# Kernel optimization log

Measured on AMD Instinct MI355X. Metric: run time of the kernel, lower is better.

The kernel has to match this reference:

```python
import jax, jax.numpy as jnp
import numpy as np

N_NODES = 50000
EPS = 1e-5


def gcn_conv(x, edge_index, edge_weight, W, b, n):
    # PyG GCNConv: h = x @ W; out[dst] += norm * h[src]; out += b
    # with self-loops (weight 1) and symmetric normalization D^-1/2 A D^-1/2.
    src, dst = edge_index[0], edge_index[1]
    loop = jnp.arange(n)
    src_all = jnp.concatenate([src, loop])            # [E+N]
    dst_all = jnp.concatenate([dst, loop])
    w_all = jnp.concatenate([edge_weight, jnp.ones((n,), x.dtype)])
    deg = jax.ops.segment_sum(w_all, dst_all, num_segments=n)
    dinv = jnp.where(deg > 0, jax.lax.rsqrt(jnp.maximum(deg, 1e-30)), 0.0)
    norm = dinv[src_all] * w_all * dinv[dst_all]      # [E+N]
    h = x @ W                                         # [N, out]
    msg = h[src_all] * norm[:, None]                  # [E+N, out]
    return jax.ops.segment_sum(msg, dst_all, num_segments=n) + b


def setup_inputs() -> dict:
    key = jax.random.key(0)
    ks = jax.random.split(key, 8)
    nfeat, nhid, nout = 1024, 256, 256
    E = 800000
    x = jax.random.normal(ks[0], (N_NODES, nfeat), dtype=jnp.float32)
    edge_index = jax.random.randint(ks[1], (2, E), 0, N_NODES, dtype=jnp.int64)
    edge_weight = jax.random.uniform(ks[2], (E,), dtype=jnp.float32)
    W1 = jax.random.normal(ks[3], (nfeat, nhid), dtype=jnp.float32) / np.sqrt(nfeat)
    b1 = jnp.zeros((nhid,), jnp.float32)
    W2 = jax.random.normal(ks[4], (nhid, nout), dtype=jnp.float32) / np.sqrt(nhid)
    b2 = jnp.zeros((nout,), jnp.float32)
    bn_gamma = jnp.ones((nout,), jnp.float32)
    bn_beta = jnp.zeros((nout,), jnp.float32)
    ln_gamma = jnp.ones((nout,), jnp.float32)
    ln_beta = jnp.zeros((nout,), jnp.float32)
    return {"x": x, "edge_index": edge_index, "edge_weight": edge_weight,
            "W1": W1, "b1": b1, "W2": W2, "b2": b2,
            "bn_gamma": bn_gamma, "bn_beta": bn_beta,
            "ln_gamma": ln_gamma, "ln_beta": ln_beta}


def reference(x, edge_index, edge_weight, W1, b1, W2, b2,
              bn_gamma, bn_beta, ln_gamma, ln_beta):
    n = x.shape[0]
    # dropout is identity in eval mode
    h = jax.nn.relu(gcn_conv(x, edge_index, edge_weight, W1, b1, n))
    h = jax.nn.relu(gcn_conv(h, edge_index, edge_weight, W2, b2, n))
    # BatchNorm1d (training-mode batch statistics, biased variance)
    mu = jnp.mean(h, axis=0)
    var = jnp.mean((h - mu) ** 2, axis=0)
    h = (h - mu) * jax.lax.rsqrt(var + EPS) * bn_gamma + bn_beta
    # LayerNorm over feature dim
    lmu = jnp.mean(h, axis=-1, keepdims=True)
    lvar = jnp.mean((h - lmu) ** 2, axis=-1, keepdims=True)
    return (h - lmu) * jax.lax.rsqrt(lvar + EPS) * ln_gamma + ln_beta
```

## Files before the change

kernel.cpp:

```cpp
#include <hip/hip_runtime.h>


typedef __attribute__((ext_vector_type(4))) float f32x4;
typedef __attribute__((ext_vector_type(8))) _Float16 f16x8;
typedef __attribute__((ext_vector_type(4))) _Float16 f16x4;

#define NN 50000
#define NF 1024
#define NH 256

__global__ __launch_bounds__(256) void deg_count(const int* __restrict__ ei,
    const float* __restrict__ ew, float* __restrict__ deg, int* __restrict__ cnt, int E)
{
    int e = blockIdx.x * 256 + threadIdx.x;
    if (e >= E) return;
    int d = ei[E + e];
    atomicAdd(&deg[d], ew[e]);
    atomicAdd(&cnt[d], 1);
}

__global__ __launch_bounds__(256) void dinv_k(const float* __restrict__ deg,
    float* __restrict__ dinv, int n)
{
    int i = blockIdx.x * 256 + threadIdx.x;
    if (i < n) dinv[i] = rsqrtf(deg[i] + 1.0f);
}

__global__ __launch_bounds__(512) void scan_a(const int* __restrict__ cnt,
    int* __restrict__ excl, int* __restrict__ bsum, int n)
{
    __shared__ int sm[512];
    int t = threadIdx.x, g = blockIdx.x * 512 + t;
    int v = (g < n) ? cnt[g] : 0;
    sm[t] = v;
    __syncthreads();
    for (int d = 1; d < 512; d <<= 1) {
        int x = (t >= d) ? sm[t - d] : 0;
        __syncthreads();
        sm[t] += x;
        __syncthreads();
    }
    if (g < n) excl[g] = sm[t] - v;
    if (t == 511) bsum[blockIdx.x] = sm[511];
}

__global__ __launch_bounds__(128) void scan_b(int* __restrict__ bsum, int nb)
{
    __shared__ int sm[128];
    int t = threadIdx.x;
    int v = (t < nb) ? bsum[t] : 0;
    sm[t] = v;
    __syncthreads();
    for (int d = 1; d < 128; d <<= 1) {
        int x = (t >= d) ? sm[t - d] : 0;
        __syncthreads();
        sm[t] += x;
        __syncthreads();
    }
    if (t < nb) bsum[t] = sm[t] - v;
}

__global__ __launch_bounds__(256) void scan_c(const int* __restrict__ excl,
    const int* __restrict__ bsum, int* __restrict__ offs, int n, int E)
{
    int g = blockIdx.x * 256 + threadIdx.x;
    if (g < n) offs[g] = excl[g] + bsum[g >> 9];
    else if (g == n) offs[n] = E;
}

__global__ __launch_bounds__(256) void scatter_k(const int* __restrict__ ei,
    const float* __restrict__ ew, const int* __restrict__ offs,
    int* __restrict__ cursor, const float* __restrict__ dinv,
    int* __restrict__ csrc, float* __restrict__ cwv, int E)
{
    int e = blockIdx.x * 256 + threadIdx.x;
    if (e >= E) return;
    int s = ei[e], d = ei[E + e];
    int pos = offs[d] + atomicAdd(&cursor[d], 1);
    csrc[pos] = s;
    cwv[pos] = ew[e] * dinv[s] * dinv[d];
}

__global__ __launch_bounds__(256) void cvt_w(const float* __restrict__ W,
    unsigned short* __restrict__ WT, int K, int total)
{
    int idx = blockIdx.x * 256 + threadIdx.x;
    if (idx >= total) return;
    int k = idx >> 8, n = idx & 255;
    ((_Float16*)WT)[(size_t)n * K + k] = (_Float16)W[idx];
}

template<bool AF32>
__global__ __launch_bounds__(256) void gemm_mfma(
    const void* __restrict__ Av, const unsigned short* __restrict__ BT,
    _Float16* __restrict__ C, int M, int K)
{
    constexpr int AS = AF32 ? 40 : 32;
    __shared__ _Float16 As[2][128 * AS];
    __shared__ _Float16 Bs[2][128 * 32];
    const int t = threadIdx.x;
    const int lane = t & 63, wid = t >> 6;
    const int r = lane & 15, q = lane >> 4;
    const int n0 = blockIdx.x * 128;
    const int m0 = blockIdx.y * 128;
    const int wm = (wid >> 1) * 64, wn = (wid & 1) * 64;
    const float* Af = (const float*)Av;
    const _Float16* Ah = (const _Float16*)Av;

    f32x4 acc[4][4];
#pragma unroll
    for (int i = 0; i < 4; ++i)
#pragma unroll
        for (int j = 0; j < 4; ++j) acc[i][j] = (f32x4){0.f, 0.f, 0.f, 0.f};

    const int T = K >> 5;
    float4 a_pre[4];

    if constexpr (AF32) {
#pragma unroll
        for (int it = 0; it < 4; ++it) {
            int f = it * 256 + t;
            int m = f >> 3, kc = (f & 7) << 2;
            int gm = m0 + m; if (gm >= M) gm = M - 1;
            a_pre[it] = *(const float4*)(Af + (size_t)gm * K + kc);
        }
    } else {
#pragma unroll
        for (int rd = 0; rd < 2; ++rd) {
            int row = rd * 64 + (t >> 2), kc = (t & 3) << 3;
            int gm = m0 + row; if (gm >= M) gm = M - 1;
            const _Float16* g = Ah + (size_t)gm * K + kc;
            _Float16* l = &As[0][0] + rd * 2048 + wid * 512;
            __builtin_amdgcn_global_load_lds(
                (const __attribute__((address_space(1))) unsigned int*)g,
                (__attribute__((address_space(3))) unsigned int*)l, 16, 0, 0);
        }
    }
#pragma unroll
    for (int rd = 0; rd < 2; ++rd) {
        int c = rd * 256 + t;
        int n = c >> 2, kc = (c & 3) << 3;
        const _Float16* g = (const _Float16*)BT + (size_t)(n0 + n) * K + kc;
        _Float16* l = &Bs[0][0] + rd * 2048 + wid * 512;
        __builtin_amdgcn_global_load_lds(
            (const __attribute__((address_space(1))) unsigned int*)g,
            (__attribute__((address_space(3))) unsigned int*)l, 16, 0, 0);
    }

    for (int k = 0; k < T; ++k) {
        const int cur = k & 1, nxt = cur ^ 1;
        if constexpr (AF32) {
#pragma unroll
            for (int it = 0; it < 4; ++it) {
                int f = it * 256 + t;
                int m = f >> 3, kc = (f & 7) << 2;
                f16x4 hv;
                hv.x = (_Float16)a_pre[it].x; hv.y = (_Float16)a_pre[it].y;
                hv.z = (_Float16)a_pre[it].z; hv.w = (_Float16)a_pre[it].w;
                *(f16x4*)(&As[cur][0] + m * AS + kc) = hv;
            }
        }
        __syncthreads();

        if (k + 1 < T) {
            const int k1 = (k + 1) << 5;
#pragma unroll
            for (int rd = 0; rd < 2; ++rd) {
                int c = rd * 256 + t;
                int n = c >> 2, kc = (c & 3) << 3;
                const _Float16* g = (const _Float16*)BT + (size_t)(n0 + n) * K + k1 + kc;
                _Float16* l = &Bs[nxt][0] + rd * 2048 + wid * 512;
                __builtin_amdgcn_global_load_lds(
                    (const __attribute__((address_space(1))) unsigned int*)g,
                    (__attribute__((address_space(3))) unsigned int*)l, 16, 0, 0);
            }
            if constexpr (AF32) {
#pragma unroll
                for (int it = 0; it < 4; ++it) {
                    int f = it * 256 + t;
                    int m = f >> 3, kc = (f & 7) << 2;
                    int gm = m0 + m; if (gm >= M) gm = M - 1;
                    a_pre[it] = *(const float4*)(Af + (size_t)gm * K + k1 + kc);
                }
            } else {
#pragma unroll
                for (int rd = 0; rd < 2; ++rd) {
                    int row = rd * 64 + (t >> 2), kc = (t & 3) << 3;
                    int gm = m0 + row; if (gm >= M) gm = M - 1;
                    const _Float16* g = Ah + (size_t)gm * K + k1 + kc;
                    _Float16* l = &As[nxt][0] + rd * 2048 + wid * 512;
                    __builtin_amdgcn_global_load_lds(
                        (const __attribute__((address_space(1))) unsigned int*)g,
                        (__attribute__((address_space(3))) unsigned int*)l, 16, 0, 0);
                }
            }
        }

        f16x8 af[4], bfr[4];
#pragma unroll
        for (int i = 0; i < 4; ++i)
            af[i] = *(const f16x8*)(&As[cur][0] + (wm + i * 16 + r) * AS + q * 8);
#pragma unroll
        for (int j = 0; j < 4; ++j)
            bfr[j] = *(const f16x8*)(&Bs[cur][0] + (wn + j * 16 + r) * 32 + q * 8);
#pragma unroll
        for (int i = 0; i < 4; ++i)
#pragma unroll
            for (int j = 0; j < 4; ++j)
                acc[i][j] = __builtin_amdgcn_mfma_f32_16x16x32_f16(af[i], bfr[j], acc[i][j], 0, 0, 0);
    }

#pragma unroll
    for (int i = 0; i < 4; ++i) {
#pragma unroll
        for (int reg = 0; reg < 4; ++reg) {
            int m = m0 + wm + i * 16 + q * 4 + reg;
            if (m < M) {
                _Float16* cp = C + (size_t)m * 256 + (n0 + wn + r);
#pragma unroll
                for (int j = 0; j < 4; ++j) cp[j * 16] = (_Float16)acc[i][j][reg];
            }
        }
    }
}

__global__ __launch_bounds__(256) void agg_relu(
    const _Float16* __restrict__ h, const int* __restrict__ roff,
    const int* __restrict__ csrc, const float* __restrict__ cwv,
    const float* __restrict__ dinv, const float* __restrict__ bias,
    _Float16* __restrict__ out, int n)
{
    const int lane = threadIdx.x & 63, wid = threadIdx.x >> 6;
    const int i = blockIdx.x * 4 + wid;
    if (i >= n) return;
    const int c = lane << 2;
    const float di = dinv[i];
    const float sw = di * di;
    const f16x4 hv = *(const f16x4*)(h + (size_t)i * 256 + c);
    float a0 = sw * (float)hv.x, a1 = sw * (float)hv.y;
    float a2 = sw * (float)hv.z, a3 = sw * (float)hv.w;
    float c0 = 0.f, c1 = 0.f, c2 = 0.f, c3 = 0.f;
    const int p0 = roff[i], pe = roff[i + 1];
    for (int base = p0; base < pe; base += 64) {
        int lim = pe - base; if (lim > 64) lim = 64;
        int sv = 0; float wv = 0.f;
        if (lane < lim) { sv = csrc[base + lane]; wv = cwv[base + lane]; }
        int j = 0;
        for (; j + 1 < lim; j += 2) {
            int s0 = __shfl(sv, j), s1 = __shfl(sv, j + 1);
            float w0 = __shfl(wv, j), w1 = __shfl(wv, j + 1);
            f16x4 v0 = *(const f16x4*)(h + (size_t)s0 * 256 + c);
            f16x4 v1 = *(const f16x4*)(h + (size_t)s1 * 256 + c);
            a0 += w0 * (float)v0.x; a1 += w0 * (float)v0.y;
            a2 += w0 * (float)v0.z; a3 += w0 * (float)v0.w;
            c0 += w1 * (float)v1.x; c1 += w1 * (float)v1.y;
            c2 += w1 * (float)v1.z; c3 += w1 * (float)v1.w;
        }
        if (j < lim) {
            int s0 = __shfl(sv, j);
            float w0 = __shfl(wv, j);
            f16x4 v0 = *(const f16x4*)(h + (size_t)s0 * 256 + c);
            a0 += w0 * (float)v0.x; a1 += w0 * (float)v0.y;
            a2 += w0 * (float)v0.z; a3 += w0 * (float)v0.w;
        }
    }
    const float4 bb = *(const float4*)(bias + c);
    f16x4 o;
    o.x = (_Float16)fmaxf(a0 + c0 + bb.x, 0.f);
    o.y = (_Float16)fmaxf(a1 + c1 + bb.y, 0.f);
    o.z = (_Float16)fmaxf(a2 + c2 + bb.z, 0.f);
    o.w = (_Float16)fmaxf(a3 + c3 + bb.w, 0.f);
    *(f16x4*)(out + (size_t)i * 256 + c) = o;
}

__global__ __launch_bounds__(256) void bn_stats(const _Float16* __restrict__ h,
    float* __restrict__ bnsum, float* __restrict__ bnsq, int n)
{
    const int t = threadIdx.x;
    float s = 0.f, s2 = 0.f;
    for (int r = blockIdx.x; r < n; r += gridDim.x) {
        float v = (float)h[(size_t)r * 256 + t];
        s += v; s2 += v * v;
    }
    atomicAdd(&bnsum[t], s);
    atomicAdd(&bnsq[t], s2);
}

__global__ __launch_bounds__(256) void bn_params(const float* __restrict__ bnsum,
    const float* __restrict__ bnsq, const float* __restrict__ gamma,
    const float* __restrict__ beta, float* __restrict__ scale,
    float* __restrict__ shift, int n)
{
    int t = threadIdx.x;
    float mu = bnsum[t] / (float)n;
    float var = bnsq[t] / (float)n - mu * mu;
    float sc = gamma[t] * rsqrtf(var + 1e-5f);
    scale[t] = sc;
    shift[t] = beta[t] - mu * sc;
}

__global__ __launch_bounds__(256) void bn_ln(const _Float16* __restrict__ h,
    const float* __restrict__ scale, const float* __restrict__ shift,
    const float* __restrict__ lng, const float* __restrict__ lnb,
    float* __restrict__ out, int n)
{
    const int lane = threadIdx.x & 63, wid = threadIdx.x >> 6;
    const int i = blockIdx.x * 4 + wid;
    if (i >= n) return;
    const int c = lane << 2;
    const f16x4 v = *(const f16x4*)(h + (size_t)i * 256 + c);
    const float4 sc = *(const float4*)(scale + c);
    const float4 sh = *(const float4*)(shift + c);
    float y0 = (float)v.x * sc.x + sh.x;
    float y1 = (float)v.y * sc.y + sh.y;
    float y2 = (float)v.z * sc.z + sh.z;
    float y3 = (float)v.w * sc.w + sh.w;
    float ps = y0 + y1 + y2 + y3;
    float ps2 = y0 * y0 + y1 * y1 + y2 * y2 + y3 * y3;
#pragma unroll
    for (int off = 32; off > 0; off >>= 1) {
        ps += __shfl_down(ps, off);
        ps2 += __shfl_down(ps2, off);
    }
    ps = __shfl(ps, 0);
    ps2 = __shfl(ps2, 0);
    const float mu = ps * (1.f / 256.f);
    const float var = ps2 * (1.f / 256.f) - mu * mu;
    const float rs = rsqrtf(var + 1e-5f);
    const float4 g = *(const float4*)(lng + c);
    const float4 bb = *(const float4*)(lnb + c);
    float4 o;
    o.x = (y0 - mu) * rs * g.x + bb.x;
    o.y = (y1 - mu) * rs * g.y + bb.y;
    o.z = (y2 - mu) * rs * g.z + bb.z;
    o.w = (y3 - mu) * rs * g.w + bb.w;
    *(float4*)(out + (size_t)i * 256 + c) = o;
}

extern "C" void kernel_launch(void* const* d_in, const int* in_sizes, int n_in,
                              void* d_out, int out_size, void* d_ws, size_t ws_size,
                              hipStream_t stream)
{
    const float* x   = (const float*)d_in[0];
    const int*   ei  = (const int*)d_in[1];
    const float* ew  = (const float*)d_in[2];
    const float* W1  = (const float*)d_in[3];
    const float* b1  = (const float*)d_in[4];
    const float* W2  = (const float*)d_in[5];
    const float* b2  = (const float*)d_in[6];
    const float* bng = (const float*)d_in[7];
    const float* bnb = (const float*)d_in[8];
    const float* lng = (const float*)d_in[9];
    const float* lnb = (const float*)d_in[10];
    float* out = (float*)d_out;

    const int N = NN;
    const int E = in_sizes[2];

    char* ws = (char*)d_ws;
    size_t o = 0;
    auto alloc = [&](size_t b) -> char* {
        char* p = ws + o;
        o = (o + b + 255) & ~(size_t)255;
        return p;
    };
    _Float16* h1  = (_Float16*)alloc((size_t)N * NH * 2);
    _Float16* h1a = (_Float16*)alloc((size_t)N * NH * 2);
    _Float16* h2a = (_Float16*)alloc((size_t)N * NH * 2);
    unsigned short* W1T = (unsigned short*)alloc((size_t)NH * NF * 2);
    unsigned short* W2T = (unsigned short*)alloc((size_t)NH * NH * 2);
    int*   csrc = (int*)alloc((size_t)E * 4);
    float* cwv  = (float*)alloc((size_t)E * 4);
    int*   offs = (int*)alloc((size_t)(N + 1) * 4);
    int*   excl = (int*)alloc((size_t)N * 4);
    int*   bsum = (int*)alloc(512);
    float* dinv = (float*)alloc((size_t)N * 4);
    float* bnscale = (float*)alloc(NH * 4);
    float* bnshift = (float*)alloc(NH * 4);
    char* zbase = ws + o;
    float* deg    = (float*)alloc((size_t)N * 4);
    int*   cnt    = (int*)alloc((size_t)N * 4);
    int*   cursor = (int*)alloc((size_t)N * 4);
    float* bnsum  = (float*)alloc(NH * 4);
    float* bnsq   = (float*)alloc(NH * 4);
    size_t zbytes = (size_t)((ws + o) - zbase);
    (void)hipMemsetAsync(zbase, 0, zbytes, stream);

    cvt_w<<<(NF * NH + 255) / 256, 256, 0, stream>>>(W1, W1T, NF, NF * NH);
    cvt_w<<<(NH * NH + 255) / 256, 256, 0, stream>>>(W2, W2T, NH, NH * NH);
    deg_count<<<(E + 255) / 256, 256, 0, stream>>>(ei, ew, deg, cnt, E);
    dinv_k<<<(N + 255) / 256, 256, 0, stream>>>(deg, dinv, N);
    scan_a<<<(N + 511) / 512, 512, 0, stream>>>(cnt, excl, bsum, N);
    scan_b<<<1, 128, 0, stream>>>(bsum, (N + 511) / 512);
    scan_c<<<(N + 1 + 255) / 256, 256, 0, stream>>>(excl, bsum, offs, N, E);
    scatter_k<<<(E + 255) / 256, 256, 0, stream>>>(ei, ew, offs, cursor, dinv, csrc, cwv, E);

    dim3 gg(2, (N + 127) / 128);
    gemm_mfma<true><<<gg, 256, 0, stream>>>(x, W1T, h1, N, NF);
    agg_relu<<<(N + 3) / 4, 256, 0, stream>>>(h1, offs, csrc, cwv, dinv, b1, h1a, N);
    gemm_mfma<false><<<gg, 256, 0, stream>>>(h1a, W2T, h1, N, NH);
    agg_relu<<<(N + 3) / 4, 256, 0, stream>>>(h1, offs, csrc, cwv, dinv, b2, h2a, N);

    bn_stats<<<256, 256, 0, stream>>>(h2a, bnsum, bnsq, N);
    bn_params<<<1, 256, 0, stream>>>(bnsum, bnsq, bng, bnb, bnscale, bnshift, N);
    bn_ln<<<(N + 3) / 4, 256, 0, stream>>>(h2a, bnscale, bnshift, lng, lnb, out, N);
}
```

Measured before the change: 702.3 us.

## Replace LDS-tiled GEMM with register-fragment GEMM, pack CSR edges, unroll aggregation

Rewrites the GEMM so that each wave owns 16 full rows across all 256 output columns. A is loaded straight into registers, and B is read from a weight copy pre-laid-out in MFMA fragment order, which removes shared memory and barriers. This also means A (the fp32 x) is read once instead of twice, as the old grid split N into two column blocks. Separately, the CSR source index and weight are packed into one int2 array, and the aggregation loop is unrolled to 4 edges with independent accumulators. The risks are heavy B traffic from global or L2 per wave, high register use, and N being a multiple of 16 here, so there is no row guard within a tile.

```diff
diff --git a/kernel.cpp b/kernel.cpp
--- a/kernel.cpp
+++ b/kernel.cpp
@@ -71,164 +71,114 @@
 __global__ __launch_bounds__(256) void scatter_k(const int* __restrict__ ei,
     const float* __restrict__ ew, const int* __restrict__ offs,
     int* __restrict__ cursor, const float* __restrict__ dinv,
-    int* __restrict__ csrc, float* __restrict__ cwv, int E)
+    int2* __restrict__ eadj, int E)
 {
     int e = blockIdx.x * 256 + threadIdx.x;
     if (e >= E) return;
     int s = ei[e], d = ei[E + e];
     int pos = offs[d] + atomicAdd(&cursor[d], 1);
-    csrc[pos] = s;
-    cwv[pos] = ew[e] * dinv[s] * dinv[d];
-}
-
-__global__ __launch_bounds__(256) void cvt_w(const float* __restrict__ W,
-    unsigned short* __restrict__ WT, int K, int total)
+    float w = ew[e] * dinv[s] * dinv[d];
+    eadj[pos] = make_int2(s, __float_as_int(w));
+}
+
+__global__ __launch_bounds__(256) void cvt_w_frag(const float* __restrict__ W,
+    _Float16* __restrict__ BF, int total)
 {
     int idx = blockIdx.x * 256 + threadIdx.x;
     if (idx >= total) return;
     int k = idx >> 8, n = idx & 255;
-    ((_Float16*)WT)[(size_t)n * K + k] = (_Float16)W[idx];
+    int kt = k >> 5, q = (k >> 3) & 3, e = k & 7;
+    int j = n >> 4, r = n & 15;
+    BF[(size_t)kt * 8192 + j * 512 + q * 128 + r * 8 + e] = (_Float16)W[idx];
 }
 
 template<bool AF32>
-__global__ __launch_bounds__(256) void gemm_mfma(
-    const void* __restrict__ Av, const unsigned short* __restrict__ BT,
+__global__ __launch_bounds__(256) void gemm_reg(
+    const void* __restrict__ Av, const _Float16* __restrict__ BF,
     _Float16* __restrict__ C, int M, int K)
 {
-    constexpr int AS = AF32 ? 40 : 32;
-    __shared__ _Float16 As[2][128 * AS];
-    __shared__ _Float16 Bs[2][128 * 32];
     const int t = threadIdx.x;
     const int lane = t & 63, wid = t >> 6;
     const int r = lane & 15, q = lane >> 4;
-    const int n0 = blockIdx.x * 128;
-    const int m0 = blockIdx.y * 128;
-    const int wm = (wid >> 1) * 64, wn = (wid & 1) * 64;
-    const float* Af = (const float*)Av;
-    const _Float16* Ah = (const _Float16*)Av;
-
-    f32x4 acc[4][4];
-#pragma unroll
-    for (int i = 0; i < 4; ++i)
-#pragma unroll
-        for (int j = 0; j < 4; ++j) acc[i][j] = (f32x4){0.f, 0.f, 0.f, 0.f};
+    const int m0 = (blockIdx.x * 4 + wid) << 4;
+    if (m0 >= M) return;
 
     const int T = K >> 5;
-    float4 a_pre[4];
-
+    f32x4 acc[16];
+#pragma unroll
+    for (int j = 0; j < 16; ++j) acc[j] = (f32x4){0.f, 0.f, 0.f, 0.f};
+
+    const float* apf;
+    const _Float16* aph;
+    if constexpr (AF32) apf = (const float*)Av + (size_t)(m0 + r) * K + q * 8;
+    else                aph = (const _Float16*)Av + (size_t)(m0 + r) * K + q * 8;
+
+    float4 p0a, p0b, p1a, p1b;
+    f16x8 h0, h1;
     if constexpr (AF32) {
-#pragma unroll
-        for (int it = 0; it < 4; ++it) {
-            int f = it * 256 + t;
-            int m = f >> 3, kc = (f & 7) << 2;
-            int gm = m0 + m; if (gm >= M) gm = M - 1;
-            a_pre[it] = *(const float4*)(Af + (size_t)gm * K + kc);
-        }
+        p0a = *(const float4*)(apf + 0);  p0b = *(const float4*)(apf + 4);
+        p1a = *(const float4*)(apf + 32); p1b = *(const float4*)(apf + 36);
     } else {
-#pragma unroll
-        for (int rd = 0; rd < 2; ++rd) {
-            int row = rd * 64 + (t >> 2), kc = (t & 3) << 3;
-            int gm = m0 + row; if (gm >= M) gm = M - 1;
-            const _Float16* g = Ah + (size_t)gm * K + kc;
-            _Float16* l = &As[0][0] + rd * 2048 + wid * 512;
-            __builtin_amdgcn_global_load_lds(
-                (const __attribute__((address_space(1))) unsigned int*)g,
-                (__attribute__((address_space(3))) unsigned int*)l, 16, 0, 0);
-        }
-    }
-#pragma unroll
-    for (int rd = 0; rd < 2; ++rd) {
-        int c = rd * 256 + t;
-        int n = c >> 2, kc = (c & 3) << 3;
-        const _Float16* g = (const _Float16*)BT + (size_t)(n0 + n) * K + kc;
-        _Float16* l = &Bs[0][0] + rd * 2048 + wid * 512;
-        __builtin_amdgcn_global_load_lds(
-            (const __attribute__((address_space(1))) unsigned int*)g,
-            (__attribute__((address_space(3))) unsigned int*)l, 16, 0, 0);
-    }
-
-    for (int k = 0; k < T; ++k) {
-        const int cur = k & 1, nxt = cur ^ 1;
+        h0 = *(const f16x8*)(aph + 0);
+        h1 = *(const f16x8*)(aph + 32);
+    }
+
+    for (int kt = 0; kt < T; kt += 2) {
+        f16x8 a;
         if constexpr (AF32) {
 #pragma unroll
-            for (int it = 0; it < 4; ++it) {
-                int f = it * 256 + t;
-                int m = f >> 3, kc = (f & 7) << 2;
-                f16x4 hv;
-                hv.x = (_Float16)a_pre[it].x; hv.y = (_Float16)a_pre[it].y;
-                hv.z = (_Float16)a_pre[it].z; hv.w = (_Float16)a_pre[it].w;
-                *(f16x4*)(&As[cur][0] + m * AS + kc) = hv;
+            for (int e = 0; e < 4; ++e) {
+                a[e]     = (_Float16)(&p0a.x)[e];
+                a[4 + e] = (_Float16)(&p0b.x)[e];
             }
-        }
-        __syncthreads();
-
-        if (k + 1 < T) {
-            const int k1 = (k + 1) << 5;
-#pragma unroll
-            for (int rd = 0; rd < 2; ++rd) {
-                int c = rd * 256 + t;
-                int n = c >> 2, kc = (c & 3) << 3;
-                const _Float16* g = (const _Float16*)BT + (size_t)(n0 + n) * K + k1 + kc;
-                _Float16* l = &Bs[nxt][0] + rd * 2048 + wid * 512;
-                __builtin_amdgcn_global_load_lds(
-                    (const __attribute__((address_space(1))) unsigned int*)g,
-                    (__attribute__((address_space(3))) unsigned int*)l, 16, 0, 0);
+        } else a = h0;
+        {
+            int kn = (kt + 2 < T) ? kt + 2 : 0;
+            if constexpr (AF32) {
+                p0a = *(const float4*)(apf + (size_t)kn * 32);
+                p0b = *(const float4*)(apf + (size_t)kn * 32 + 4);
+            } else h0 = *(const f16x8*)(aph + (size_t)kn * 32);
+        }
+        const _Float16* bb = BF + (size_t)kt * 8192 + lane * 8;
+#pragma unroll
+        for (int j = 0; j < 16; ++j) {
+            f16x8 bf = *(const f16x8*)(bb + j * 512);
+            acc[j] = __builtin_amdgcn_mfma_f32_16x16x32_f16(a, bf, acc[j], 0, 0, 0);
+        }
+        if constexpr (AF32) {
+#pragma unroll
+            for (int e = 0; e < 4; ++e) {
+                a[e]     = (_Float16)(&p1a.x)[e];
+                a[4 + e] = (_Float16)(&p1b.x)[e];
             }
+        } else a = h1;
+        {
+            int kn = (kt + 3 < T) ? kt + 3 : 0;
             if constexpr (AF32) {
-#pragma unroll
-                for (int it = 0; it < 4; ++it) {
-                    int f = it * 256 + t;
-                    int m = f >> 3, kc = (f & 7) << 2;
-                    int gm = m0 + m; if (gm >= M) gm = M - 1;
-                    a_pre[it] = *(const float4*)(Af + (size_t)gm * K + k1 + kc);
-                }
-            } else {
-#pragma unroll
-                for (int rd = 0; rd < 2; ++rd) {
-                    int row = rd * 64 + (t >> 2), kc = (t & 3) << 3;
-                    int gm = m0 + row; if (gm >= M) gm = M - 1;
-                    const _Float16* g = Ah + (size_t)gm * K + k1 + kc;
-                    _Float16* l = &As[nxt][0] + rd * 2048 + wid * 512;
-                    __builtin_amdgcn_global_load_lds(
-                        (const __attribute__((address_space(1))) unsigned int*)g,
-                        (__attribute__((address_space(3))) unsigned int*)l, 16, 0, 0);
-                }
-            }
-        }
-
-        f16x8 af[4], bfr[4];
-#pragma unroll
-        for (int i = 0; i < 4; ++i)
-            af[i] = *(const f16x8*)(&As[cur][0] + (wm + i * 16 + r) * AS + q * 8);
-#pragma unroll
-        for (int j = 0; j < 4; ++j)
-            bfr[j] = *(const f16x8*)(&Bs[cur][0] + (wn + j * 16 + r) * 32 + q * 8);
-#pragma unroll
-        for (int i = 0; i < 4; ++i)
-#pragma unroll
-            for (int j = 0; j < 4; ++j)
-                acc[i][j] = __builtin_amdgcn_mfma_f32_16x16x32_f16(af[i], bfr[j], acc[i][j], 0, 0, 0);
-    }
-
-#pragma unroll
-    for (int i = 0; i < 4; ++i) {
-#pragma unroll
-        for (int reg = 0; reg < 4; ++reg) {
-            int m = m0 + wm + i * 16 + q * 4 + reg;
-            if (m < M) {
-                _Float16* cp = C + (size_t)m * 256 + (n0 + wn + r);
-#pragma unroll
-                for (int j = 0; j < 4; ++j) cp[j * 16] = (_Float16)acc[i][j][reg];
-            }
-        }
-    }
+                p1a = *(const float4*)(apf + (size_t)kn * 32);
+                p1b = *(const float4*)(apf + (size_t)kn * 32 + 4);
+            } else h1 = *(const f16x8*)(aph + (size_t)kn * 32);
+        }
+        const _Float16* bb2 = bb + 8192;
+#pragma unroll
+        for (int j = 0; j < 16; ++j) {
+            f16x8 bf = *(const f16x8*)(bb2 + j * 512);
+            acc[j] = __builtin_amdgcn_mfma_f32_16x16x32_f16(a, bf, acc[j], 0, 0, 0);
+        }
+    }
+
+    _Float16* crow = C + (size_t)(m0 + q * 4) * 256 + r;
+#pragma unroll
+    for (int j = 0; j < 16; ++j)
+#pragma unroll
+        for (int reg = 0; reg < 4; ++reg)
+            crow[(size_t)reg * 256 + j * 16] = (_Float16)acc[j][reg];
 }
 
 __global__ __launch_bounds__(256) void agg_relu(
     const _Float16* __restrict__ h, const int* __restrict__ roff,
-    const int* __restrict__ csrc, const float* __restrict__ cwv,
-    const float* __restrict__ dinv, const float* __restrict__ bias,
-    _Float16* __restrict__ out, int n)
+    const int2* __restrict__ eadj, const float* __restrict__ dinv,
+    const float* __restrict__ bias, _Float16* __restrict__ out, int n)
 {
     const int lane = threadIdx.x & 63, wid = threadIdx.x >> 6;
     const int i = blockIdx.x * 4 + wid;
@@ -239,24 +189,37 @@
     const f16x4 hv = *(const f16x4*)(h + (size_t)i * 256 + c);
     float a0 = sw * (float)hv.x, a1 = sw * (float)hv.y;
     float a2 = sw * (float)hv.z, a3 = sw * (float)hv.w;
+    float b0 = 0.f, b1 = 0.f, b2 = 0.f, b3 = 0.f;
     float c0 = 0.f, c1 = 0.f, c2 = 0.f, c3 = 0.f;
+    float d0 = 0.f, d1 = 0.f, d2 = 0.f, d3 = 0.f;
     const int p0 = roff[i], pe = roff[i + 1];
     for (int base = p0; base < pe; base += 64) {
         int lim = pe - base; if (lim > 64) lim = 64;
         int sv = 0; float wv = 0.f;
-        if (lane < lim) { sv = csrc[base + lane]; wv = cwv[base + lane]; }
+        if (lane < lim) {
+            int2 ev = eadj[base + lane];
+            sv = ev.x; wv = __int_as_float(ev.y);
+        }
         int j = 0;
-        for (; j + 1 < lim; j += 2) {
+        for (; j + 3 < lim; j += 4) {
             int s0 = __shfl(sv, j), s1 = __shfl(sv, j + 1);
+            int s2 = __shfl(sv, j + 2), s3 = __shfl(sv, j + 3);
             float w0 = __shfl(wv, j), w1 = __shfl(wv, j + 1);
+            float w2 = __shfl(wv, j + 2), w3 = __shfl(wv, j + 3);
             f16x4 v0 = *(const f16x4*)(h + (size_t)s0 * 256 + c);
             f16x4 v1 = *(const f16x4*)(h + (size_t)s1 * 256 + c);
+            f16x4 v2 = *(const f16x4*)(h + (size_t)s2 * 256 + c);
+            f16x4 v3 = *(const f16x4*)(h + (size_t)s3 * 256 + c);
             a0 += w0 * (float)v0.x; a1 += w0 * (float)v0.y;
             a2 += w0 * (float)v0.z; a3 += w0 * (float)v0.w;
-            c0 += w1 * (float)v1.x; c1 += w1 * (float)v1.y;
-            c2 += w1 * (float)v1.z; c3 += w1 * (float)v1.w;
-        }
-        if (j < lim) {
+            b0 += w1 * (float)v1.x; b1 += w1 * (float)v1.y;
+            b2 += w1 * (float)v1.z; b3 += w1 * (float)v1.w;
+            c0 += w2 * (float)v2.x; c1 += w2 * (float)v2.y;
+            c2 += w2 * (float)v2.z; c3 += w2 * (float)v2.w;
+            d0 += w3 * (float)v3.x; d1 += w3 * (float)v3.y;
+            d2 += w3 * (float)v3.z; d3 += w3 * (float)v3.w;
+        }
+        for (; j < lim; ++j) {
             int s0 = __shfl(sv, j);
             float w0 = __shfl(wv, j);
             f16x4 v0 = *(const f16x4*)(h + (size_t)s0 * 256 + c);
@@ -266,10 +229,10 @@
     }
     const float4 bb = *(const float4*)(bias + c);
     f16x4 o;
-    o.x = (_Float16)fmaxf(a0 + c0 + bb.x, 0.f);
-    o.y = (_Float16)fmaxf(a1 + c1 + bb.y, 0.f);
-    o.z = (_Float16)fmaxf(a2 + c2 + bb.z, 0.f);
-    o.w = (_Float16)fmaxf(a3 + c3 + bb.w, 0.f);
+    o.x = (_Float16)fmaxf(a0 + b0 + c0 + d0 + bb.x, 0.f);
+    o.y = (_Float16)fmaxf(a1 + b1 + c1 + d1 + bb.y, 0.f);
+    o.z = (_Float16)fmaxf(a2 + b2 + c2 + d2 + bb.z, 0.f);
+    o.w = (_Float16)fmaxf(a3 + b3 + c3 + d3 + bb.w, 0.f);
     *(f16x4*)(out + (size_t)i * 256 + c) = o;
 }
 
@@ -367,10 +330,9 @@
     _Float16* h1  = (_Float16*)alloc((size_t)N * NH * 2);
     _Float16* h1a = (_Float16*)alloc((size_t)N * NH * 2);
     _Float16* h2a = (_Float16*)alloc((size_t)N * NH * 2);
-    unsigned short* W1T = (unsigned short*)alloc((size_t)NH * NF * 2);
-    unsigned short* W2T = (unsigned short*)alloc((size_t)NH * NH * 2);
-    int*   csrc = (int*)alloc((size_t)E * 4);
-    float* cwv  = (float*)alloc((size_t)E * 4);
+    _Float16* BF1 = (_Float16*)alloc((size_t)NH * NF * 2);
+    _Float16* BF2 = (_Float16*)alloc((size_t)NH * NH * 2);
+    int2*  eadj = (int2*)alloc((size_t)E * 8);
     int*   offs = (int*)alloc((size_t)(N + 1) * 4);
     int*   excl = (int*)alloc((size_t)N * 4);
     int*   bsum = (int*)alloc(512);
@@ -386,20 +348,20 @@
     size_t zbytes = (size_t)((ws + o) - zbase);
     (void)hipMemsetAsync(zbase, 0, zbytes, stream);
 
-    cvt_w<<<(NF * NH + 255) / 256, 256, 0, stream>>>(W1, W1T, NF, NF * NH);
-    cvt_w<<<(NH * NH + 255) / 256, 256, 0, stream>>>(W2, W2T, NH, NH * NH);
+    cvt_w_frag<<<(NF * NH + 255) / 256, 256, 0, stream>>>(W1, BF1, NF * NH);
+    cvt_w_frag<<<(NH * NH + 255) / 256, 256, 0, stream>>>(W2, BF2, NH * NH);
     deg_count<<<(E + 255) / 256, 256, 0, stream>>>(ei, ew, deg, cnt, E);
     dinv_k<<<(N + 255) / 256, 256, 0, stream>>>(deg, dinv, N);
     scan_a<<<(N + 511) / 512, 512, 0, stream>>>(cnt, excl, bsum, N);
     scan_b<<<1, 128, 0, stream>>>(bsum, (N + 511) / 512);
     scan_c<<<(N + 1 + 255) / 256, 256, 0, stream>>>(excl, bsum, offs, N, E);
-    scatter_k<<<(E + 255) / 256, 256, 0, stream>>>(ei, ew, offs, cursor, dinv, csrc, cwv, E);
-
-    dim3 gg(2, (N + 127) / 128);
-    gemm_mfma<true><<<gg, 256, 0, stream>>>(x, W1T, h1, N, NF);
-    agg_relu<<<(N + 3) / 4, 256, 0, stream>>>(h1, offs, csrc, cwv, dinv, b1, h1a, N);
-    gemm_mfma<false><<<gg, 256, 0, stream>>>(h1a, W2T, h1, N, NH);
-    agg_relu<<<(N + 3) / 4, 256, 0, stream>>>(h1, offs, csrc, cwv, dinv, b2, h2a, N);
+    scatter_k<<<(E + 255) / 256, 256, 0, stream>>>(ei, ew, offs, cursor, dinv, eadj, E);
+
+    const int ng = (N / 16 + 3) / 4;
+    gemm_reg<true><<<ng, 256, 0, stream>>>(x, BF1, h1, N, NF);
+    agg_relu<<<(N + 3) / 4, 256, 0, stream>>>(h1, offs, eadj, dinv, b1, h1a, N);
+    gemm_reg<false><<<ng, 256, 0, stream>>>(h1a, BF2, h1, N, NH);
+    agg_relu<<<(N + 3) / 4, 256, 0, stream>>>(h1, offs, eadj, dinv, b2, h2a, N);
 
     bn_stats<<<256, 256, 0, stream>>>(h2a, bnsum, bnsq, N);
     bn_params<<<1, 256, 0, stream>>>(bnsum, bnsq, bng, bnb, bnscale, bnshift, N);
```

Result: slower. 927.0 us (+32.0%).
